# Kernel optimization log

Hardware: AMD Instinct MI355X
Metric: run time of the kernel (lower is better)

## Reference

```python
import jax, jax.numpy as jnp
import numpy as np

B, Cin, H, W = 8, 256, 32, 32
KS, NH, K = 32, 8, 5          # key_size == value_size, num_heads, kernel_size
STRIDE, PAD = 1, 2
Cout = KS * 3 * NH            # 768
EPS = 1e-5


def setup_inputs() -> dict:
    key = jax.random.key(0)
    k0, k1, k2 = jax.random.split(key, 3)
    return {
        "x": jax.random.normal(k0, (B, Cin, H, W), jnp.float32),
        "conv_w": jax.random.normal(k1, (Cout, Cin), jnp.float32) / np.sqrt(Cin).astype(np.float32),
        "conv_b": jax.random.normal(k2, (Cout,), jnp.float32) * 0.02,
        "gn_w": jnp.ones((Cout,), jnp.float32),
        "gn_b": jnp.zeros((Cout,), jnp.float32),
    }


def reference(x, conv_w, conv_b, gn_w, gn_b):
    Bb = x.shape[0]
    OH = (H + 2 * PAD - K) // STRIDE + 1
    OW = (W + 2 * PAD - K) // STRIDE + 1

    # 1x1 conv: (B, Cout, H, W)
    attn = jnp.einsum('bchw,oc->bohw', x, conv_w) + conv_b[None, :, None, None]

    # unfold / Tile2d -> (B, KH, KW, Cout, OH, OW)
    ap = jnp.pad(attn, ((0, 0), (0, 0), (PAD, PAD), (PAD, PAD)))
    rows = []
    for kh in range(K):
        cols = [ap[:, :, kh:kh + OH * STRIDE:STRIDE, kw:kw + OW * STRIDE:STRIDE]
                for kw in range(K)]
        rows.append(jnp.stack(cols, axis=1))          # (B, KW, C, OH, OW)
    tiles = jnp.stack(rows, axis=1)                   # (B, KH, KW, C, OH, OW)

    # GroupNorm over (group_channels, OH, OW) per (b, kh, kw) sample.
    # groups = 3*NH, group size = KS (each head's key/query/value chunk).
    G = 3 * NH
    t = tiles.reshape(Bb, K, K, G, KS, OH, OW)
    mean = t.mean(axis=(4, 5, 6), keepdims=True)
    var = t.var(axis=(4, 5, 6), keepdims=True)        # biased, like torch GroupNorm
    t = (t - mean) * jax.lax.rsqrt(var + EPS)
    t = t.reshape(Bb, K, K, Cout, OH, OW)
    t = t * gn_w[None, None, None, :, None, None] + gn_b[None, None, None, :, None, None]

    # (B, OH, OW, NH, 3*KS, KH*KW)
    t = t.transpose(0, 4, 5, 3, 1, 2).reshape(Bb, OH, OW, NH, 3 * KS, K * K)
    keyt = t[..., :KS, :]            # (B, OH, OW, NH, KS, KK)
    qt = t[..., KS:2 * KS, :]
    vt = t[..., 2 * KS:, :]          # (B, OH, OW, NH, VS, KK)

    q = qt.mean(axis=-1)             # mean query over the window: (B, OH, OW, NH, KS)
    sal = jnp.einsum('bijnk,bijnkp->bijnp', q, keyt) / np.float32(np.sqrt(KS))
    mask = jax.nn.softmax(sal, axis=-1)               # (B, OH, OW, NH, KK)
    out = jnp.einsum('bijnvp,bijnp->bijnv', vt, mask)  # (B, OH, OW, NH, VS)

    out = out.transpose(0, 3, 4, 1, 2).reshape(Bb, NH * KS, OH, OW)
    return out
```

## Files before the change

kernel.cpp:

```cpp
#include <hip/hip_runtime.h>
#include <hip/hip_bf16.h>

#define B_    8
#define CIN   256
#define COUT  768
#define G_    24
#define PW    40
#define PLANE 1440
#define EPS_  1e-5f

typedef float f32x4 __attribute__((ext_vector_type(4)));
typedef short s16x8 __attribute__((ext_vector_type(8)));
typedef unsigned short ushort_t;
typedef unsigned short u16x4 __attribute__((ext_vector_type(4)));
typedef unsigned long long ull_t;

#define LDS_FENCE() do { asm volatile("" ::: "memory"); \
                         __builtin_amdgcn_s_waitcnt(0xC07F); \
                         asm volatile("" ::: "memory"); } while (0)

static __device__ __forceinline__ ushort_t f2bf(float f) {
    union { float f; unsigned u; } a; a.f = f;
    const unsigned u = a.u;
    const unsigned r = u + 0x7FFFu + ((u >> 16) & 1u);
    return (ushort_t)(r >> 16);
}
static __device__ __forceinline__ float bf2f(ushort_t h) {
    union { unsigned u; float f; } a; a.u = ((unsigned)h) << 16; return a.f;
}
static __device__ __forceinline__ void st4(float* dst, u16x4 v) {
    *(f32x4*)dst = f32x4{ bf2f(v[0]), bf2f(v[1]), bf2f(v[2]), bf2f(v[3]) };
}
static __device__ __forceinline__ unsigned pk2(float lo, float hi) {
    return (unsigned)f2bf(lo) | ((unsigned)f2bf(hi) << 16);
}

__launch_bounds__(256)
__global__ void conv_gemm(const float* __restrict__ wsrc, const float* __restrict__ x,
                          const float* __restrict__ bias, ushort_t* __restrict__ attn,
                          float* __restrict__ rowAgg) {
    const int t = threadIdx.x;
    const int wv = t >> 6, lane = t & 63;
    const int q = lane >> 4, l15 = lane & 15;
    const int m0 = blockIdx.y * 64;
    const int mw = wv * 16;
    const int n_t = blockIdx.x * 64;
    const int b = n_t >> 10, nl0 = n_t & 1023;
    const int y0 = nl0 >> 5;

    __shared__ ushort_t Bs[64][264];
    ushort_t (*Ct)[2][44] = (ushort_t (*)[2][44])(&Bs[0][0]);
    float (*red)[11]      = (float (*)[11])((char*)(&Bs[0][0]) + 64 * 2 * 44 * 2);

    {
        const int half = t >> 7;
        const int kp = t & 127;
        const int k2 = kp * 2;
        const float* xr0 = x + (size_t)b * (CIN * 1024) + (size_t)k2 * 1024 + nl0 + half * 32;
        const float* xr1 = xr0 + 1024;
        #pragma unroll
        for (int c = 0; c < 8; ++c) {
            const float4 u0 = *(const float4*)(xr0 + c * 4);
            const float4 u1 = *(const float4*)(xr1 + c * 4);
            const int nn = half * 32 + c * 4;
            *(unsigned*)&Bs[nn + 0][k2] = pk2(u0.x, u1.x);
            *(unsigned*)&Bs[nn + 1][k2] = pk2(u0.y, u1.y);
            *(unsigned*)&Bs[nn + 2][k2] = pk2(u0.z, u1.z);
            *(unsigned*)&Bs[nn + 3][k2] = pk2(u0.w, u1.w);
        }
    }
    __syncthreads();

    const float* aPf = wsrc + (size_t)(m0 + mw + l15) * 256 + q * 8;

    f32x4 acc[4] = {{0,0,0,0},{0,0,0,0},{0,0,0,0},{0,0,0,0}};
    #pragma unroll
    for (int k0 = 0; k0 < 256; k0 += 32) {
        const float4 af0 = *(const float4*)(aPf + k0);
        const float4 af1 = *(const float4*)(aPf + k0 + 4);
        s16x8 a;
        a[0] = (short)f2bf(af0.x); a[1] = (short)f2bf(af0.y);
        a[2] = (short)f2bf(af0.z); a[3] = (short)f2bf(af0.w);
        a[4] = (short)f2bf(af1.x); a[5] = (short)f2bf(af1.y);
        a[6] = (short)f2bf(af1.z); a[7] = (short)f2bf(af1.w);
        const int kk = k0 + q * 8;
        const s16x8 b0 = *(const s16x8*)&Bs[l15 +  0][kk];
        const s16x8 b1 = *(const s16x8*)&Bs[l15 + 16][kk];
        const s16x8 b2 = *(const s16x8*)&Bs[l15 + 32][kk];
        const s16x8 b3 = *(const s16x8*)&Bs[l15 + 48][kk];
        acc[0] = __builtin_amdgcn_mfma_f32_16x16x32_bf16(a, b0, acc[0], 0, 0, 0);
        acc[1] = __builtin_amdgcn_mfma_f32_16x16x32_bf16(a, b1, acc[1], 0, 0, 0);
        acc[2] = __builtin_amdgcn_mfma_f32_16x16x32_bf16(a, b2, acc[2], 0, 0, 0);
        acc[3] = __builtin_amdgcn_mfma_f32_16x16x32_bf16(a, b3, acc[3], 0, 0, 0);
    }
    __syncthreads();

    float bb[4];
    #pragma unroll
    for (int r = 0; r < 4; ++r) bb[r] = bias[m0 + mw + q * 4 + r];
    #pragma unroll
    for (int j = 0; j < 4; ++j) {
        const int yy = j >> 1, xx = (j & 1) * 16 + l15;
        #pragma unroll
        for (int r = 0; r < 4; ++r)
            Ct[mw + q * 4 + r][yy][2 + xx] = f2bf(acc[j][r] + bb[r]);
    }
    #pragma unroll
    for (int it = 0; it < 2; ++it) {
        const int id = it * 256 + t;
        const int m = id >> 3, yy = (id >> 2) & 1, pos = id & 3;
        const int us = (pos == 0) ? 0 : (32 + 2 * pos);
        *(unsigned*)&Ct[m][yy][us] = 0u;
    }
    __syncthreads();

    ushort_t* pb = attn + ((size_t)(b * COUT + m0)) * PLANE;
    #pragma unroll
    for (int it = 0; it < 5; ++it) {
        const int id = it * 256 + t;
        const int m = id / 20, rem = id % 20, yy = rem / 10, s = rem % 10;
        const ull_t v = *(const ull_t*)&Ct[m][yy][s * 4];
        *(ull_t*)(pb + (size_t)m * PLANE + (y0 + yy + 2) * PW + s * 4) = v;
    }
    if (y0 == 0 || y0 == 30) {
        const int rowA = (y0 == 0) ? 0 : 34;
        #pragma unroll
        for (int it = 0; it < 5; ++it) {
            const int id = it * 256 + t;
            const int m = id / 20, rem = id % 20, yy = rem / 10, s = rem % 10;
            *(ull_t*)(pb + (size_t)m * PLANE + (rowA + yy) * PW + s * 4) = 0ull;
        }
    }

    if (t < 128) {
        const int gi = t >> 6, yy = (t >> 5) & 1, c = t & 31;
        const int m = gi * 32 + c;
        float lin = 0.f, sq = 0.f, e0 = 0.f, e1 = 0.f, e30 = 0.f, e31 = 0.f;
        #pragma unroll
        for (int u = 0; u < 9; ++u) {
            const ull_t vv = *(const ull_t*)&Ct[m][yy][u * 4];
            const unsigned lo = (unsigned)vv, hi = (unsigned)(vv >> 32);
            union { unsigned u; float f; } f0, f1, f2, f3;
            f0.u = lo << 16; f1.u = lo & 0xffff0000u;
            f2.u = hi << 16; f3.u = hi & 0xffff0000u;
            lin += (f0.f + f1.f) + (f2.f + f3.f);
            sq  += (f0.f * f0.f + f1.f * f1.f) + (f2.f * f2.f + f3.f * f3.f);
            if (u == 0) { e0 = f2.f; e1 = f3.f; }
            if (u == 8) { e30 = f0.f; e31 = f1.f; }
        }
        red[t][0] = lin; red[t][1] = sq;
        red[t][2] = e0;  red[t][3] = e0 * e0;
        red[t][4] = e1;  red[t][5] = e1 * e1;
        red[t][6] = e30; red[t][7] = e30 * e30;
        red[t][8] = e31; red[t][9] = e31 * e31;
    }
    __syncthreads();
    if (t < 40) {
        const int s = t % 10, gy = t / 10;
        const int gi = gy >> 1, yy = gy & 1;
        float sum = 0.f;
        #pragma unroll
        for (int c = 0; c < 32; ++c) sum += red[gi * 64 + yy * 32 + c][s];
        const int g = blockIdx.y * 2 + gi;
        rowAgg[(((size_t)b * G_ + g) * 32 + (y0 + yy)) * 10 + s] = sum;
    }
}

__launch_bounds__(64)
__global__ void gnfin(const float* __restrict__ rowAgg,
                      float* __restrict__ meanArr, float* __restrict__ rstdArr) {
    const int bg = blockIdx.x;
    const int t = threadIdx.x;
    __shared__ float rp[32][5], rp2[32][5];
    if (t < 32) {
        const float* a = rowAgg + ((size_t)bg * 32 + t) * 10;
        const float S = a[0], Sq = a[1];
        const float e0 = a[2], q0 = a[3], e1 = a[4], q1 = a[5];
        const float e30 = a[6], q30 = a[7], e31 = a[8], q31 = a[9];
        rp[t][0] = S - e30 - e31; rp[t][1] = S - e31; rp[t][2] = S;
        rp[t][3] = S - e0;        rp[t][4] = S - e0 - e1;
        rp2[t][0] = Sq - q30 - q31; rp2[t][1] = Sq - q31; rp2[t][2] = Sq;
        rp2[t][3] = Sq - q0;        rp2[t][4] = Sq - q0 - q1;
    }
    __syncthreads();
    if (t < 25) {
        const int kw = t % 5, kh = t / 5;
        float cs = 0.f, cs2 = 0.f;
        #pragma unroll
        for (int yy = 0; yy < 32; ++yy) { cs += rp[yy][kw]; cs2 += rp2[yy][kw]; }
        if (kh == 0)      { cs -= rp[30][kw] + rp[31][kw]; cs2 -= rp2[30][kw] + rp2[31][kw]; }
        else if (kh == 1) { cs -= rp[31][kw];              cs2 -= rp2[31][kw]; }
        else if (kh == 3) { cs -= rp[0][kw];               cs2 -= rp2[0][kw]; }
        else if (kh == 4) { cs -= rp[0][kw] + rp[1][kw];   cs2 -= rp2[0][kw] + rp2[1][kw]; }
        const float inv_n = 1.f / 32768.f;
        const float mean = cs * inv_n;
        const float var  = cs2 * inv_n - mean * mean;
        meanArr[bg * 25 + t] = mean;
        rstdArr[bg * 25 + t] = rsqrtf(var + EPS_);
    }
}

__launch_bounds__(64)
__global__ void local_attn(const ushort_t* __restrict__ attn,
                           const float* __restrict__ meanArr, const float* __restrict__ rstdArr,
                           const float* __restrict__ gn_w, const float* __restrict__ gn_b,
                           float* __restrict__ out) {
    const int blk = blockIdx.x;
    const int b = blk >> 8;
    const int n = (blk >> 5) & 7;
    const int i0 = blk & 31;
    const int t = threadIdx.x;
    const int h = t >> 5;
    const int j = t & 31;

    __shared__ float KB[2][2][208];
    __shared__ float QB[2][2][208];
    __shared__ float s_rq[25], s_mq[25], s_rk[25], s_ck[25], s_rv[25], s_cv[25];
    __shared__ float s_gw[96], s_gb[96];

    if (t < 25) {
        const int gk = (b * G_ + n * 3) * 25 + t;
        const float mK = meanArr[gk],      rK = rstdArr[gk];
        const float mQ = meanArr[gk + 25], rQ = rstdArr[gk + 25];
        const float mV = meanArr[gk + 50], rV = rstdArr[gk + 50];
        s_rk[t] = rK; s_ck[t] = mK * rK;
        s_rq[t] = rQ; s_mq[t] = mQ * rQ;
        s_rv[t] = rV; s_cv[t] = mV * rV;
    }
    s_gw[t] = gn_w[n * 96 + t];
    s_gb[t] = gn_b[n * 96 + t];
    if (t < 32) {
        s_gw[64 + t] = gn_w[n * 96 + 64 + t];
        s_gb[64 + t] = gn_b[n * 96 + 64 + t];
    }
    __syncthreads();

    float rq[25]; float cQ = 0.f;
    #pragma unroll
    for (int p = 0; p < 25; ++p) { rq[p] = s_rq[p]; cQ += s_mq[p]; }

    const ushort_t* regB = attn + (size_t)(b * COUT + n * 96) * PLANE + i0 * PW;
    const bool stg = (j < 25);
    const int eo1 = j * 4, eo2 = (j + 25) * 4;

    const ushort_t* baseK = regB + (size_t)(h * 16) * PLANE;
    const ushort_t* baseQ = regB + (size_t)(32 + h * 16) * PLANE;
    const ushort_t* baseV = regB + (size_t)(64 + h * 16) * PLANE;

    u16x4 nK1{0,0,0,0}, nK2{0,0,0,0}, nQ1{0,0,0,0}, nQ2{0,0,0,0};
    u16x4 fK1{0,0,0,0}, fK2{0,0,0,0}, fQ1{0,0,0,0}, fQ2{0,0,0,0};
    if (stg) {
        const u16x4 a1 = *(const u16x4*)(baseK + eo1), a2 = *(const u16x4*)(baseK + eo2);
        const u16x4 q1 = *(const u16x4*)(baseQ + eo1), q2 = *(const u16x4*)(baseQ + eo2);
        st4(&KB[h][0][eo1], a1); st4(&KB[h][0][eo2], a2);
        st4(&QB[h][0][eo1], q1); st4(&QB[h][0][eo2], q2);
        nK1 = *(const u16x4*)(baseK + PLANE + eo1); nK2 = *(const u16x4*)(baseK + PLANE + eo2);
        nQ1 = *(const u16x4*)(baseQ + PLANE + eo1); nQ2 = *(const u16x4*)(baseQ + PLANE + eo2);
        fK1 = *(const u16x4*)(baseK + 2 * (size_t)PLANE + eo1);
        fK2 = *(const u16x4*)(baseK + 2 * (size_t)PLANE + eo2);
        fQ1 = *(const u16x4*)(baseQ + 2 * (size_t)PLANE + eo1);
        fQ2 = *(const u16x4*)(baseQ + 2 * (size_t)PLANE + eo2);
    }
    LDS_FENCE();

    float sal[25];
    #pragma unroll
    for (int p = 0; p < 25; ++p) sal[p] = 0.f;
    float sumQ2 = 0.f, sumQB = 0.f;

    for (int cc = 0; cc < 16; ++cc) {
        const int buf = cc & 1;
        if (stg && cc < 15) {
            st4(&KB[h][buf ^ 1][eo1], nK1); st4(&KB[h][buf ^ 1][eo2], nK2);
            st4(&QB[h][buf ^ 1][eo1], nQ1); st4(&QB[h][buf ^ 1][eo2], nQ2);
            nK1 = fK1; nK2 = fK2; nQ1 = fQ1; nQ2 = fQ2;
            if (cc < 13) {
                fK1 = *(const u16x4*)(baseK + (size_t)(cc + 3) * PLANE + eo1);
                fK2 = *(const u16x4*)(baseK + (size_t)(cc + 3) * PLANE + eo2);
                fQ1 = *(const u16x4*)(baseQ + (size_t)(cc + 3) * PLANE + eo1);
                fQ2 = *(const u16x4*)(baseQ + (size_t)(cc + 3) * PLANE + eo2);
            } else if (cc == 13) {
                fK1 = *(const u16x4*)(baseV + eo1);
                fK2 = *(const u16x4*)(baseV + eo2);
                fQ1 = *(const u16x4*)(baseV + (size_t)PLANE + eo1);
                fQ2 = *(const u16x4*)(baseV + (size_t)PLANE + eo2);
            }
        }
        const int ch = h * 16 + cc;
        const float* qb = &QB[h][buf][j];
        const float* kb = &KB[h][buf][j];
        float qa0 = 0.f, qa1 = 0.f, qa2 = 0.f, qa3 = 0.f, qa4 = 0.f;
        #pragma unroll
        for (int kw = 0; kw < 5; ++kw) {
            qa0 += rq[0 * 5 + kw] * qb[0 * PW + kw];
            qa1 += rq[1 * 5 + kw] * qb[1 * PW + kw];
            qa2 += rq[2 * 5 + kw] * qb[2 * PW + kw];
            qa3 += rq[3 * 5 + kw] * qb[3 * PW + kw];
            qa4 += rq[4 * 5 + kw] * qb[4 * PW + kw];
        }
        const float qa = (qa0 + qa1) + (qa2 + qa3) + qa4;
        const float qk  = s_gw[32 + ch] * ((qa - cQ) * 0.04f) + s_gb[32 + ch];
        const float qk2 = qk * s_gw[ch];
        sumQ2 += qk2; sumQB += qk * s_gb[ch];
        #pragma unroll
        for (int kh = 0; kh < 5; ++kh)
            #pragma unroll
            for (int kw = 0; kw < 5; ++kw)
                sal[kh * 5 + kw] += qk2 * kb[kh * PW + kw];
        LDS_FENCE();
    }

    u16x4 vA1 = nQ1, vA2 = nQ2, vB1{0,0,0,0}, vB2{0,0,0,0};
    if (stg) {
        st4(&KB[h][0][eo1], nK1); st4(&KB[h][0][eo2], nK2);
        vB1 = *(const u16x4*)(baseV + 2 * (size_t)PLANE + eo1);
        vB2 = *(const u16x4*)(baseV + 2 * (size_t)PLANE + eo2);
    }

    sumQ2 += __shfl_xor(sumQ2, 32);
    sumQB += __shfl_xor(sumQB, 32);
    #pragma unroll
    for (int p = 0; p < 25; ++p) sal[p] += __shfl_xor(sal[p], 32);

    #pragma unroll
    for (int p = 0; p < 25; ++p) sal[p] = s_rk[p] * sal[p] - s_ck[p] * sumQ2 + sumQB;

    const float scale = 0.17677669529663687f;
    float mmax = -3.4e38f;
    #pragma unroll
    for (int p = 0; p < 25; ++p) { sal[p] *= scale; mmax = fmaxf(mmax, sal[p]); }
    float ssum = 0.f;
    #pragma unroll
    for (int p = 0; p < 25; ++p) { sal[p] = __expf(sal[p] - mmax); ssum += sal[p]; }
    const float rs = 1.f / ssum;
    float cV2 = 0.f;
    #pragma unroll
    for (int p = 0; p < 25; ++p) {
        const float m = sal[p] * rs;
        sal[p] = m * s_rv[p];
        cV2 += m * s_cv[p];
    }
    LDS_FENCE();

    for (int cc = 0; cc < 16; ++cc) {
        const int buf = cc & 1;
        if (stg && cc < 15) {
            st4(&KB[h][buf ^ 1][eo1], vA1); st4(&KB[h][buf ^ 1][eo2], vA2);
            vA1 = vB1; vA2 = vB2;
            if (cc < 13) {
                vB1 = *(const u16x4*)(baseV + (size_t)(cc + 3) * PLANE + eo1);
                vB2 = *(const u16x4*)(baseV + (size_t)(cc + 3) * PLANE + eo2);
            }
        }
        const int v = h * 16 + cc;
        const float* vb = &KB[h][buf][j];
        float a0 = 0.f, a1 = 0.f, a2 = 0.f, a3 = 0.f, a4 = 0.f;
        #pragma unroll
        for (int kw = 0; kw < 5; ++kw) {
            a0 += sal[0 * 5 + kw] * vb[0 * PW + kw];
            a1 += sal[1 * 5 + kw] * vb[1 * PW + kw];
            a2 += sal[2 * 5 + kw] * vb[2 * PW + kw];
            a3 += sal[3 * 5 + kw] * vb[3 * PW + kw];
            a4 += sal[4 * 5 + kw] * vb[4 * PW + kw];
        }
        const float acc = (a0 + a1) + (a2 + a3) + a4;
        out[((size_t)(b * 256 + n * 32 + v) * 32 + i0) * 32 + j] =
            s_gw[64 + v] * acc + (s_gb[64 + v] - s_gw[64 + v] * cV2);
        LDS_FENCE();
    }
}

extern "C" void kernel_launch(void* const* d_in, const int* in_sizes, int n_in,
                              void* d_out, int out_size, void* d_ws, size_t ws_size,
                              hipStream_t stream) {
    const float* x      = (const float*)d_in[0];
    const float* conv_w = (const float*)d_in[1];
    const float* conv_b = (const float*)d_in[2];
    const float* gn_w   = (const float*)d_in[3];
    const float* gn_b   = (const float*)d_in[4];
    float* out = (float*)d_out;

    ushort_t* attn    = (ushort_t*)d_ws;
    float*    rowAgg  = (float*)(attn + 8847360);
    float*    meanArr = rowAgg + 61440;
    float*    rstdArr = meanArr + 4800;

    conv_gemm<<<dim3(128, 12), 256, 0, stream>>>(conv_w, x, conv_b, attn, rowAgg);
    gnfin<<<192, 64, 0, stream>>>(rowAgg, meanArr, rstdArr);
    local_attn<<<2048, 64, 0, stream>>>(attn, meanArr, rstdArr, gn_w, gn_b, out);
}
```

Measured before the change: 122.3 us.

## Fuse GroupNorm finalize into local attention and swizzle block order

Removes the separate gnfin kernel launch. Each local_attn block now recomputes the mean and rstd for its three groups from rowAgg in shared memory. This drops one launch and a global round-trip, but adds redundant per-block reduction work and two extra syncs. The block index is also remapped so that consecutive blocks span different batches, which changes how work is spread across CUs and how cache locality behaves.

Measured after the change: 131.3 us. +7.3%, slower.

```diff
diff --git a/kernel.cpp b/kernel.cpp
--- a/kernel.cpp
+++ b/kernel.cpp
@@ -167,71 +167,80 @@
 }
 
 __launch_bounds__(64)
-__global__ void gnfin(const float* __restrict__ rowAgg,
-                      float* __restrict__ meanArr, float* __restrict__ rstdArr) {
-    const int bg = blockIdx.x;
-    const int t = threadIdx.x;
-    __shared__ float rp[32][5], rp2[32][5];
-    if (t < 32) {
-        const float* a = rowAgg + ((size_t)bg * 32 + t) * 10;
-        const float S = a[0], Sq = a[1];
-        const float e0 = a[2], q0 = a[3], e1 = a[4], q1 = a[5];
-        const float e30 = a[6], q30 = a[7], e31 = a[8], q31 = a[9];
-        rp[t][0] = S - e30 - e31; rp[t][1] = S - e31; rp[t][2] = S;
-        rp[t][3] = S - e0;        rp[t][4] = S - e0 - e1;
-        rp2[t][0] = Sq - q30 - q31; rp2[t][1] = Sq - q31; rp2[t][2] = Sq;
-        rp2[t][3] = Sq - q0;        rp2[t][4] = Sq - q0 - q1;
-    }
-    __syncthreads();
-    if (t < 25) {
-        const int kw = t % 5, kh = t / 5;
-        float cs = 0.f, cs2 = 0.f;
-        #pragma unroll
-        for (int yy = 0; yy < 32; ++yy) { cs += rp[yy][kw]; cs2 += rp2[yy][kw]; }
-        if (kh == 0)      { cs -= rp[30][kw] + rp[31][kw]; cs2 -= rp2[30][kw] + rp2[31][kw]; }
-        else if (kh == 1) { cs -= rp[31][kw];              cs2 -= rp2[31][kw]; }
-        else if (kh == 3) { cs -= rp[0][kw];               cs2 -= rp2[0][kw]; }
-        else if (kh == 4) { cs -= rp[0][kw] + rp[1][kw];   cs2 -= rp2[0][kw] + rp2[1][kw]; }
-        const float inv_n = 1.f / 32768.f;
-        const float mean = cs * inv_n;
-        const float var  = cs2 * inv_n - mean * mean;
-        meanArr[bg * 25 + t] = mean;
-        rstdArr[bg * 25 + t] = rsqrtf(var + EPS_);
-    }
-}
-
-__launch_bounds__(64)
 __global__ void local_attn(const ushort_t* __restrict__ attn,
-                           const float* __restrict__ meanArr, const float* __restrict__ rstdArr,
+                           const float* __restrict__ rowAgg,
                            const float* __restrict__ gn_w, const float* __restrict__ gn_b,
                            float* __restrict__ out) {
     const int blk = blockIdx.x;
-    const int b = blk >> 8;
-    const int n = (blk >> 5) & 7;
-    const int i0 = blk & 31;
+    const int wid = (blk >> 3) | ((blk & 7) << 8);
+    const int b = wid >> 8;
+    const int n = (wid >> 5) & 7;
+    const int i0 = wid & 31;
     const int t = threadIdx.x;
     const int h = t >> 5;
     const int j = t & 31;
 
     __shared__ float KB[2][2][208];
     __shared__ float QB[2][2][208];
+    __shared__ float rpL[96][5], rp2L[96][5];
+    __shared__ float s_m[75], s_r[75];
     __shared__ float s_rq[25], s_mq[25], s_rk[25], s_ck[25], s_rv[25], s_cv[25];
     __shared__ float s_gw[96], s_gb[96];
 
-    if (t < 25) {
-        const int gk = (b * G_ + n * 3) * 25 + t;
-        const float mK = meanArr[gk],      rK = rstdArr[gk];
-        const float mQ = meanArr[gk + 25], rQ = rstdArr[gk + 25];
-        const float mV = meanArr[gk + 50], rV = rstdArr[gk + 50];
-        s_rk[t] = rK; s_ck[t] = mK * rK;
-        s_rq[t] = rQ; s_mq[t] = mQ * rQ;
-        s_rv[t] = rV; s_cv[t] = mV * rV;
-    }
     s_gw[t] = gn_w[n * 96 + t];
     s_gb[t] = gn_b[n * 96 + t];
     if (t < 32) {
         s_gw[64 + t] = gn_w[n * 96 + 64 + t];
         s_gb[64 + t] = gn_b[n * 96 + 64 + t];
+    }
+
+    const float* rab = rowAgg + (size_t)((b * G_ + n * 3) * 32) * 10;
+    #pragma unroll
+    for (int pass = 0; pass < 2; ++pass) {
+        const int e = (pass == 0) ? t : 64 + t;
+        if (pass == 0 || t < 32) {
+            const float* a = rab + (size_t)e * 10;
+            const float S = a[0], Sq = a[1];
+            const float e0 = a[2], q0 = a[3], e1 = a[4], q1 = a[5];
+            const float e30 = a[6], q30 = a[7], e31 = a[8], q31 = a[9];
+            rpL[e][0] = S - e30 - e31; rpL[e][1] = S - e31; rpL[e][2] = S;
+            rpL[e][3] = S - e0;        rpL[e][4] = S - e0 - e1;
+            rp2L[e][0] = Sq - q30 - q31; rp2L[e][1] = Sq - q31; rp2L[e][2] = Sq;
+            rp2L[e][3] = Sq - q0;        rp2L[e][4] = Sq - q0 - q1;
+        }
+    }
+    __syncthreads();
+
+    #pragma unroll
+    for (int pass = 0; pass < 2; ++pass) {
+        const int e = (pass == 0) ? t : 64 + t;
+        if (e < 75) {
+            const int gi = e / 25, p = e % 25;
+            const int kw = p % 5, kh = p / 5;
+            const int rb = gi * 32;
+            float cs = 0.f, cs2 = 0.f;
+            #pragma unroll
+            for (int yy = 0; yy < 32; ++yy) { cs += rpL[rb + yy][kw]; cs2 += rp2L[rb + yy][kw]; }
+            if (kh == 0)      { cs -= rpL[rb + 30][kw] + rpL[rb + 31][kw]; cs2 -= rp2L[rb + 30][kw] + rp2L[rb + 31][kw]; }
+            else if (kh == 1) { cs -= rpL[rb + 31][kw];                    cs2 -= rp2L[rb + 31][kw]; }
+            else if (kh == 3) { cs -= rpL[rb + 0][kw];                     cs2 -= rp2L[rb + 0][kw]; }
+            else if (kh == 4) { cs -= rpL[rb + 0][kw] + rpL[rb + 1][kw];   cs2 -= rp2L[rb + 0][kw] + rp2L[rb + 1][kw]; }
+            const float inv_n = 1.f / 32768.f;
+            const float mean = cs * inv_n;
+            const float var  = cs2 * inv_n - mean * mean;
+            s_m[e] = mean;
+            s_r[e] = rsqrtf(var + EPS_);
+        }
+    }
+    __syncthreads();
+
+    if (t < 25) {
+        const float mK = s_m[t],      rK = s_r[t];
+        const float mQ = s_m[25 + t], rQ = s_r[25 + t];
+        const float mV = s_m[50 + t], rV = s_r[50 + t];
+        s_rk[t] = rK; s_ck[t] = mK * rK;
+        s_rq[t] = rQ; s_mq[t] = mQ * rQ;
+        s_rv[t] = rV; s_cv[t] = mV * rV;
     }
     __syncthreads();
 
@@ -382,10 +391,7 @@
 
     ushort_t* attn    = (ushort_t*)d_ws;
     float*    rowAgg  = (float*)(attn + 8847360);
-    float*    meanArr = rowAgg + 61440;
-    float*    rstdArr = meanArr + 4800;
 
     conv_gemm<<<dim3(128, 12), 256, 0, stream>>>(conv_w, x, conv_b, attn, rowAgg);
-    gnfin<<<192, 64, 0, stream>>>(rowAgg, meanArr, rstdArr);
-    local_attn<<<2048, 64, 0, stream>>>(attn, meanArr, rstdArr, gn_w, gn_b, out);
-}
+    local_attn<<<2048, 64, 0, stream>>>(attn, rowAgg, gn_w, gn_b, out);
+}
```
